# Performance work log

Hardware: AMD Instinct MI355X
Metric: run time of the kernel (lower is better)

Reference implementation:

```python
import jax, jax.numpy as jnp
import numpy as np

B, S, H, E = 2, 2048, 1024, 16


def setup_inputs() -> dict:
    key = jax.random.key(0)
    k0, k1, k2, k3 = jax.random.split(key, 4)
    tokens = jax.random.normal(k0, (B, S, H), dtype=jnp.float32)
    gate_w = jax.random.normal(k1, (E, H), dtype=jnp.float32) * (H ** -0.5)
    expert_w = jax.random.normal(k2, (E, H, H), dtype=jnp.float32) * (H ** -0.5)
    expert_b = jax.random.normal(k3, (E, H), dtype=jnp.float32) * 0.01
    return {"tokens": tokens, "gate_w": gate_w, "expert_w": expert_w, "expert_b": expert_b}


def reference(tokens, gate_w, expert_w, expert_b):
    b, s, h = tokens.shape
    # gate: Linear(H, E, bias=False) -> logits, softmax, top-2
    logits = jnp.einsum('bsh,eh->bse', tokens, gate_w)
    weights = jax.nn.softmax(logits, axis=-1)
    top2_w, top2_idx = jax.lax.top_k(weights, 2)           # [b,s,2]
    flat = tokens.reshape(b * s, h)                         # [N,H]
    flat_w = top2_w.reshape(b * s, 2)
    flat_idx = top2_idx.reshape(b * s, 2)
    # dense per-expert Linear+ReLU for all tokens (grouped GEMM form)
    y = jax.nn.relu(jnp.einsum('nh,edh->ned', flat, expert_w) + expert_b[None, :, :])  # [N,E,H]
    # gather the two selected experts per token and combine with gate weights
    sel = jnp.take_along_axis(y, flat_idx[:, :, None], axis=1)  # [N,2,H]
    out = jnp.sum(sel * flat_w[:, :, None], axis=1)             # [N,H]
    return out.reshape(b, s, h)
```

## Files before the change

kernel.cpp:

```cpp
#include <hip/hip_runtime.h>
#include <hip/hip_bf16.h>

#define TOKENS 4096
#define HDIM 1024
#define NEXP 16
#define BM 128
#define BN 128
#define BK 64
#define MAXMT (TOKENS / BM)

typedef __bf16 bf16x8 __attribute__((ext_vector_type(8)));
typedef __bf16 bf16x4 __attribute__((ext_vector_type(4)));
typedef float f32x4 __attribute__((ext_vector_type(4)));

__device__ inline void gload16(const void* g, const void* l) {
  __builtin_amdgcn_global_load_lds((const __attribute__((address_space(1))) void*)g,
                                   (__attribute__((address_space(3))) void*)l, 16, 0, 0);
}

#define WQ (NEXP * HDIM * HDIM / 4)
#define TQ (TOKENS * HDIM / 4)
__global__ __launch_bounds__(256) void convert_kernel(
    const float* __restrict__ w, const float* __restrict__ t,
    __bf16* __restrict__ wbf, __bf16* __restrict__ tbf) {
  int idx = blockIdx.x * 256 + threadIdx.x;
  for (int i = idx; i < WQ + TQ; i += gridDim.x * 256) {
    const float4* src;
    bf16x4* dst;
    int j;
    if (i < WQ) { src = (const float4*)w; dst = (bf16x4*)wbf; j = i; }
    else        { src = (const float4*)t; dst = (bf16x4*)tbf; j = i - WQ; }
    float4 f = src[j];
    bf16x4 v;
    v[0] = (__bf16)f.x; v[1] = (__bf16)f.y; v[2] = (__bf16)f.z; v[3] = (__bf16)f.w;
    dst[j] = v;
  }
}

__global__ __launch_bounds__(256) void gate_kernel(
    const float* __restrict__ tokens, const float* __restrict__ gate_w,
    int* __restrict__ tok_idx, float* __restrict__ tok_w) {
  int lane = threadIdx.x & 63;
  int wv = threadIdx.x >> 6;
  int token = blockIdx.x * 4 + wv;
  const float* trow = tokens + (size_t)token * HDIM;

  float4 tv[4];
#pragma unroll
  for (int s = 0; s < 4; ++s) tv[s] = *(const float4*)(trow + s * 256 + lane * 4);

  float lg[NEXP];
#pragma unroll
  for (int e = 0; e < NEXP; ++e) {
    float d = 0.f;
#pragma unroll
    for (int s = 0; s < 4; ++s) {
      float4 g = *(const float4*)(gate_w + e * HDIM + s * 256 + lane * 4);
      d += tv[s].x * g.x + tv[s].y * g.y + tv[s].z * g.z + tv[s].w * g.w;
    }
#pragma unroll
    for (int off = 32; off; off >>= 1) d += __shfl_xor(d, off);
    lg[e] = d;
  }

  int i0 = 0; float b0 = lg[0];
#pragma unroll
  for (int e = 1; e < NEXP; ++e) if (lg[e] > b0) { b0 = lg[e]; i0 = e; }
  int i1 = -1; float b1 = -1e30f;
#pragma unroll
  for (int e = 0; e < NEXP; ++e) {
    if (e == i0) continue;
    if (lg[e] > b1) { b1 = lg[e]; i1 = e; }
  }
  float s = 0.f;
#pragma unroll
  for (int e = 0; e < NEXP; ++e) s += expf(lg[e] - b0);
  float w0 = 1.0f / s;
  float w1 = expf(b1 - b0) / s;

  if (lane == 0) {
    tok_idx[token * 2 + 0] = i0;
    tok_idx[token * 2 + 1] = i1;
    tok_w[token * 2 + 0] = w0;
    tok_w[token * 2 + 1] = w1;
  }
}

__global__ __launch_bounds__(256) void build_lists_kernel(
    const int* __restrict__ tok_idx, const float* __restrict__ tok_w,
    int* __restrict__ counts, int* __restrict__ list_tok, float* __restrict__ list_w) {
  int e = blockIdx.x;
  __shared__ int cur;
  if (threadIdx.x == 0) cur = 0;
  __syncthreads();
  for (int s = threadIdx.x; s < TOKENS * 2; s += 256) {
    if (tok_idx[s] == e) {
      int pos = atomicAdd(&cur, 1);
      list_tok[e * TOKENS + pos] = s >> 1;
      list_w[e * TOKENS + pos] = tok_w[s];
    }
  }
  __syncthreads();
  if (threadIdx.x == 0) counts[e] = cur;
}

__global__ __launch_bounds__(256) void moe_gemm_kernel(
    const __bf16* __restrict__ tok_bf, const __bf16* __restrict__ w_bf,
    const float* __restrict__ expert_b, const int* __restrict__ counts,
    const int* __restrict__ list_tok, const float* __restrict__ list_w,
    float* __restrict__ out) {
  int e = blockIdx.x & 15;
  int mt = blockIdx.x >> 4;
  int cnt = counts[e];
  if (mt * BM >= cnt) return;
  int nt = blockIdx.y;
  const int lbase = e * TOKENS;

  __shared__ __bf16 lds[2][(BM + BN) * BK];

  int tid = threadIdx.x;
  int lane = tid & 63;
  int wv = tid >> 6;

  const __bf16* aptr[4];
  const __bf16* bptr[4];
  int dstb[4];
#pragma unroll
  for (int i = 0; i < 4; ++i) {
    int c = (wv * 4 + i) * 64 + lane;
    int r = c >> 3, kc = c & 7;
    int gr = mt * BM + r;
    int tok = list_tok[lbase + ((gr < cnt) ? gr : (cnt - 1))];
    aptr[i] = tok_bf + (size_t)tok * HDIM + (kc ^ (r & 7)) * 8;
    int d = nt * BN + r;
    bptr[i] = w_bf + (size_t)e * HDIM * HDIM + (size_t)d * HDIM + (kc ^ (r & 7)) * 8;
    dstb[i] = (wv * 4 + i) * 512;
  }

  int wr = (wv >> 1) * 64;
  int wc = (wv & 1) * 64;
  int lr = lane & 15;
  int lk = lane >> 4;

  int aoffr[2][4], boffr[2][4];
#pragma unroll
  for (int kk = 0; kk < 2; ++kk) {
#pragma unroll
    for (int m = 0; m < 4; ++m) {
      int r = wr + m * 16 + lr;
      aoffr[kk][m] = r * BK + (((kk * 4 + lk) ^ (r & 7)) * 8);
      int d = wc + m * 16 + lr;
      boffr[kk][m] = BM * BK + d * BK + (((kk * 4 + lk) ^ (d & 7)) * 8);
    }
  }

  f32x4 acc[4][4] = {};

#pragma unroll
  for (int i = 0; i < 4; ++i) gload16(aptr[i], &lds[0][dstb[i]]);
#pragma unroll
  for (int i = 0; i < 4; ++i) gload16(bptr[i], &lds[0][BM * BK + dstb[i]]);
  __syncthreads();

  int buf = 0;
  for (int kb = 0; kb < HDIM / BK; ++kb) {
    if (kb + 1 < HDIM / BK) {
      int nb = buf ^ 1;
      int ko = (kb + 1) * BK;
#pragma unroll
      for (int i = 0; i < 4; ++i) gload16(aptr[i] + ko, &lds[nb][dstb[i]]);
#pragma unroll
      for (int i = 0; i < 4; ++i) gload16(bptr[i] + ko, &lds[nb][BM * BK + dstb[i]]);
    }

    bf16x8 af[2][4], bfr[2][4];
#pragma unroll
    for (int kk = 0; kk < 2; ++kk) {
#pragma unroll
      for (int m = 0; m < 4; ++m) {
        af[kk][m] = *(const bf16x8*)(&lds[buf][aoffr[kk][m]]);
        bfr[kk][m] = *(const bf16x8*)(&lds[buf][boffr[kk][m]]);
      }
    }
#pragma unroll
    for (int kk = 0; kk < 2; ++kk)
#pragma unroll
      for (int m = 0; m < 4; ++m)
#pragma unroll
        for (int n = 0; n < 4; ++n)
          acc[m][n] = __builtin_amdgcn_mfma_f32_16x16x32_bf16(af[kk][m], bfr[kk][n], acc[m][n], 0, 0, 0);

    __syncthreads();
    buf ^= 1;
  }

#pragma unroll
  for (int m = 0; m < 4; ++m) {
#pragma unroll
    for (int j = 0; j < 4; ++j) {
      int rloc = wr + m * 16 + lk * 4 + j;
      int grow = mt * BM + rloc;
      if (grow < cnt) {
        int tok = list_tok[lbase + grow];
        float gw = list_w[lbase + grow];
        float* orow = out + (size_t)tok * HDIM + nt * BN + wc;
        const float* brow = expert_b + e * HDIM + nt * BN + wc;
#pragma unroll
        for (int n = 0; n < 4; ++n) {
          int dcol = n * 16 + lr;
          float v = acc[m][n][j] + brow[dcol];
          v = fmaxf(v, 0.f) * gw;
          atomicAdd(orow + dcol, v);
        }
      }
    }
  }
}

extern "C" void kernel_launch(void* const* d_in, const int* in_sizes, int n_in,
                              void* d_out, int out_size, void* d_ws, size_t ws_size,
                              hipStream_t stream) {
  const float* tokens = (const float*)d_in[0];
  const float* gate_w = (const float*)d_in[1];
  const float* expert_w = (const float*)d_in[2];
  const float* expert_b = (const float*)d_in[3];
  float* out = (float*)d_out;

  int* counts = (int*)d_ws;
  int* tok_idx = counts + 16;
  float* tok_w = (float*)(tok_idx + TOKENS * 2);
  int* list_tok = (int*)(tok_w + TOKENS * 2);
  float* list_w = (float*)(list_tok + NEXP * TOKENS);
  size_t head = (size_t)(list_w + NEXP * TOKENS) - (size_t)d_ws;
  head = (head + 255) & ~(size_t)255;
  __bf16* w_bf = (__bf16*)((char*)d_ws + head);
  __bf16* tok_bf = w_bf + (size_t)NEXP * HDIM * HDIM;

  hipMemsetAsync(d_out, 0, (size_t)out_size * sizeof(float), stream);

  convert_kernel<<<2048, 256, 0, stream>>>(expert_w, tokens, w_bf, tok_bf);
  gate_kernel<<<TOKENS / 4, 256, 0, stream>>>(tokens, gate_w, tok_idx, tok_w);
  build_lists_kernel<<<NEXP, 256, 0, stream>>>(tok_idx, tok_w, counts, list_tok, list_w);

  dim3 grid(NEXP * MAXMT, HDIM / BN);
  moe_gemm_kernel<<<grid, 256, 0, stream>>>(tok_bf, w_bf, expert_b, counts,
                                            list_tok, list_w, out);
}
```

Measured before the change: 236.9 us.

## Compact MoE tile schedule and use 512-thread GEMM blocks with split conversion

Adds a plan kernel that builds a compact list of (expert, m-tile) pairs, so GEMM blocks map only to real tiles instead of a sparse grid where most blocks exit early. The GEMM block grows to 512 threads (8 waves, each computing 64x32) with launch bounds for occupancy, and the fp32-to-bf16 conversion is split into two 8-wide vectorized kernels with one element group per thread. The cost is an extra single-thread serial kernel and launch, plus smaller per-wave tiles that reuse fragments less.

```diff
diff --git a/kernel.cpp b/kernel.cpp
--- a/kernel.cpp
+++ b/kernel.cpp
@@ -7,10 +7,9 @@
 #define BM 128
 #define BN 128
 #define BK 64
-#define MAXMT (TOKENS / BM)
+#define MAX_TILES (TOKENS * 2 / BM + NEXP)
 
 typedef __bf16 bf16x8 __attribute__((ext_vector_type(8)));
-typedef __bf16 bf16x4 __attribute__((ext_vector_type(4)));
 typedef float f32x4 __attribute__((ext_vector_type(4)));
 
 __device__ inline void gload16(const void* g, const void* l) {
@@ -18,23 +17,15 @@
                                    (__attribute__((address_space(3))) void*)l, 16, 0, 0);
 }
 
-#define WQ (NEXP * HDIM * HDIM / 4)
-#define TQ (TOKENS * HDIM / 4)
-__global__ __launch_bounds__(256) void convert_kernel(
-    const float* __restrict__ w, const float* __restrict__ t,
-    __bf16* __restrict__ wbf, __bf16* __restrict__ tbf) {
-  int idx = blockIdx.x * 256 + threadIdx.x;
-  for (int i = idx; i < WQ + TQ; i += gridDim.x * 256) {
-    const float4* src;
-    bf16x4* dst;
-    int j;
-    if (i < WQ) { src = (const float4*)w; dst = (bf16x4*)wbf; j = i; }
-    else        { src = (const float4*)t; dst = (bf16x4*)tbf; j = i - WQ; }
-    float4 f = src[j];
-    bf16x4 v;
-    v[0] = (__bf16)f.x; v[1] = (__bf16)f.y; v[2] = (__bf16)f.z; v[3] = (__bf16)f.w;
-    dst[j] = v;
-  }
+__global__ __launch_bounds__(256) void cvt_kernel(const float* __restrict__ src,
+                                                  __bf16* __restrict__ dst) {
+  int i = blockIdx.x * 256 + threadIdx.x;
+  float4 a = ((const float4*)src)[i * 2];
+  float4 b = ((const float4*)src)[i * 2 + 1];
+  bf16x8 v;
+  v[0] = (__bf16)a.x; v[1] = (__bf16)a.y; v[2] = (__bf16)a.z; v[3] = (__bf16)a.w;
+  v[4] = (__bf16)b.x; v[5] = (__bf16)b.y; v[6] = (__bf16)b.z; v[7] = (__bf16)b.w;
+  ((bf16x8*)dst)[i] = v;
 }
 
 __global__ __launch_bounds__(256) void gate_kernel(
@@ -104,15 +95,29 @@
   if (threadIdx.x == 0) counts[e] = cur;
 }
 
-__global__ __launch_bounds__(256) void moe_gemm_kernel(
+__global__ void plan_kernel(const int* __restrict__ counts, int* __restrict__ tiles,
+                            int* __restrict__ n_tiles) {
+  if (threadIdx.x == 0) {
+    int n = 0;
+    for (int e = 0; e < NEXP; ++e) {
+      int t = (counts[e] + BM - 1) / BM;
+      for (int m = 0; m < t; ++m) { tiles[n * 2] = e; tiles[n * 2 + 1] = m; ++n; }
+    }
+    *n_tiles = n;
+  }
+}
+
+__global__ __launch_bounds__(512, 4) void moe_gemm_kernel(
     const __bf16* __restrict__ tok_bf, const __bf16* __restrict__ w_bf,
     const float* __restrict__ expert_b, const int* __restrict__ counts,
+    const int* __restrict__ tiles, const int* __restrict__ n_tiles,
     const int* __restrict__ list_tok, const float* __restrict__ list_w,
     float* __restrict__ out) {
-  int e = blockIdx.x & 15;
-  int mt = blockIdx.x >> 4;
+  int bx = blockIdx.x;
+  if (bx >= *n_tiles) return;
+  int e = tiles[bx * 2];
+  int mt = tiles[bx * 2 + 1];
   int cnt = counts[e];
-  if (mt * BM >= cnt) return;
   int nt = blockIdx.y;
   const int lbase = e * TOKENS;
 
@@ -122,44 +127,47 @@
   int lane = tid & 63;
   int wv = tid >> 6;
 
-  const __bf16* aptr[4];
-  const __bf16* bptr[4];
-  int dstb[4];
-#pragma unroll
-  for (int i = 0; i < 4; ++i) {
-    int c = (wv * 4 + i) * 64 + lane;
+  const __bf16* aptr[2];
+  const __bf16* bptr[2];
+  int dstb[2];
+#pragma unroll
+  for (int i = 0; i < 2; ++i) {
+    int c = (wv * 2 + i) * 64 + lane;
     int r = c >> 3, kc = c & 7;
     int gr = mt * BM + r;
     int tok = list_tok[lbase + ((gr < cnt) ? gr : (cnt - 1))];
     aptr[i] = tok_bf + (size_t)tok * HDIM + (kc ^ (r & 7)) * 8;
     int d = nt * BN + r;
     bptr[i] = w_bf + (size_t)e * HDIM * HDIM + (size_t)d * HDIM + (kc ^ (r & 7)) * 8;
-    dstb[i] = (wv * 4 + i) * 512;
-  }
-
-  int wr = (wv >> 1) * 64;
-  int wc = (wv & 1) * 64;
+    dstb[i] = (wv * 2 + i) * 512;
+  }
+
+  int wr = (wv >> 2) * 64;
+  int wc = (wv & 3) * 32;
   int lr = lane & 15;
   int lk = lane >> 4;
 
-  int aoffr[2][4], boffr[2][4];
+  int aoffr[2][4], boffr[2][2];
 #pragma unroll
   for (int kk = 0; kk < 2; ++kk) {
 #pragma unroll
     for (int m = 0; m < 4; ++m) {
       int r = wr + m * 16 + lr;
       aoffr[kk][m] = r * BK + (((kk * 4 + lk) ^ (r & 7)) * 8);
-      int d = wc + m * 16 + lr;
-      boffr[kk][m] = BM * BK + d * BK + (((kk * 4 + lk) ^ (d & 7)) * 8);
-    }
-  }
-
-  f32x4 acc[4][4] = {};
-
-#pragma unroll
-  for (int i = 0; i < 4; ++i) gload16(aptr[i], &lds[0][dstb[i]]);
-#pragma unroll
-  for (int i = 0; i < 4; ++i) gload16(bptr[i], &lds[0][BM * BK + dstb[i]]);
+    }
+#pragma unroll
+    for (int n = 0; n < 2; ++n) {
+      int d = wc + n * 16 + lr;
+      boffr[kk][n] = BM * BK + d * BK + (((kk * 4 + lk) ^ (d & 7)) * 8);
+    }
+  }
+
+  f32x4 acc[4][2] = {};
+
+#pragma unroll
+  for (int i = 0; i < 2; ++i) gload16(aptr[i], &lds[0][dstb[i]]);
+#pragma unroll
+  for (int i = 0; i < 2; ++i) gload16(bptr[i], &lds[0][BM * BK + dstb[i]]);
   __syncthreads();
 
   int buf = 0;
@@ -168,26 +176,25 @@
       int nb = buf ^ 1;
       int ko = (kb + 1) * BK;
 #pragma unroll
-      for (int i = 0; i < 4; ++i) gload16(aptr[i] + ko, &lds[nb][dstb[i]]);
-#pragma unroll
-      for (int i = 0; i < 4; ++i) gload16(bptr[i] + ko, &lds[nb][BM * BK + dstb[i]]);
-    }
-
-    bf16x8 af[2][4], bfr[2][4];
+      for (int i = 0; i < 2; ++i) gload16(aptr[i] + ko, &lds[nb][dstb[i]]);
+#pragma unroll
+      for (int i = 0; i < 2; ++i) gload16(bptr[i] + ko, &lds[nb][BM * BK + dstb[i]]);
+    }
+
+    bf16x8 af[2][4], bfr[2][2];
 #pragma unroll
     for (int kk = 0; kk < 2; ++kk) {
 #pragma unroll
-      for (int m = 0; m < 4; ++m) {
-        af[kk][m] = *(const bf16x8*)(&lds[buf][aoffr[kk][m]]);
-        bfr[kk][m] = *(const bf16x8*)(&lds[buf][boffr[kk][m]]);
-      }
+      for (int m = 0; m < 4; ++m) af[kk][m] = *(const bf16x8*)(&lds[buf][aoffr[kk][m]]);
+#pragma unroll
+      for (int n = 0; n < 2; ++n) bfr[kk][n] = *(const bf16x8*)(&lds[buf][boffr[kk][n]]);
     }
 #pragma unroll
     for (int kk = 0; kk < 2; ++kk)
 #pragma unroll
       for (int m = 0; m < 4; ++m)
 #pragma unroll
-        for (int n = 0; n < 4; ++n)
+        for (int n = 0; n < 2; ++n)
           acc[m][n] = __builtin_amdgcn_mfma_f32_16x16x32_bf16(af[kk][m], bfr[kk][n], acc[m][n], 0, 0, 0);
 
     __syncthreads();
@@ -206,7 +213,7 @@
         float* orow = out + (size_t)tok * HDIM + nt * BN + wc;
         const float* brow = expert_b + e * HDIM + nt * BN + wc;
 #pragma unroll
-        for (int n = 0; n < 4; ++n) {
+        for (int n = 0; n < 2; ++n) {
           int dcol = n * 16 + lr;
           float v = acc[m][n][j] + brow[dcol];
           v = fmaxf(v, 0.f) * gw;
@@ -227,7 +234,9 @@
   float* out = (float*)d_out;
 
   int* counts = (int*)d_ws;
-  int* tok_idx = counts + 16;
+  int* n_tiles = counts + 16;
+  int* tiles = n_tiles + 16;
+  int* tok_idx = tiles + MAX_TILES * 2;
   float* tok_w = (float*)(tok_idx + TOKENS * 2);
   int* list_tok = (int*)(tok_w + TOKENS * 2);
   float* list_w = (float*)(list_tok + NEXP * TOKENS);
@@ -238,11 +247,13 @@
 
   hipMemsetAsync(d_out, 0, (size_t)out_size * sizeof(float), stream);
 
-  convert_kernel<<<2048, 256, 0, stream>>>(expert_w, tokens, w_bf, tok_bf);
+  cvt_kernel<<<NEXP * HDIM * HDIM / 8 / 256, 256, 0, stream>>>(expert_w, w_bf);
+  cvt_kernel<<<TOKENS * HDIM / 8 / 256, 256, 0, stream>>>(tokens, tok_bf);
   gate_kernel<<<TOKENS / 4, 256, 0, stream>>>(tokens, gate_w, tok_idx, tok_w);
   build_lists_kernel<<<NEXP, 256, 0, stream>>>(tok_idx, tok_w, counts, list_tok, list_w);
-
-  dim3 grid(NEXP * MAXMT, HDIM / BN);
-  moe_gemm_kernel<<<grid, 256, 0, stream>>>(tok_bf, w_bf, expert_b, counts,
+  plan_kernel<<<1, 64, 0, stream>>>(counts, tiles, n_tiles);
+
+  dim3 grid(MAX_TILES, HDIM / BN);
+  moe_gemm_kernel<<<grid, 512, 0, stream>>>(tok_bf, w_bf, expert_b, counts, tiles, n_tiles,
                                             list_tok, list_w, out);
 }
```

Result: faster. 227.7 us (-3.9%).

## Fuse weight bf16 conversion into GEMM with LDS-resident weight slab

Applied to the files above, without the earlier changes.

Removes the separate conversion kernel. The token bf16 cast moves into the gate kernel, and each GEMM block converts its own 64-column expert weight slice from fp32 into a full-K LDS slab (128KB). Each block then iterates over all of that expert's tokens, streaming A fragments straight from global memory with no LDS staging. This avoids writing and re-reading a bf16 copy of the weights, but the grid shrinks to 256 blocks, one per expert and column tile, so load imbalance across experts and uncoalesced direct A loads may limit throughput.

```diff
diff --git a/kernel.cpp b/kernel.cpp
--- a/kernel.cpp
+++ b/kernel.cpp
@@ -4,42 +4,18 @@
 #define TOKENS 4096
 #define HDIM 1024
 #define NEXP 16
-#define BM 128
-#define BN 128
-#define BK 64
-#define MAXMT (TOKENS / BM)
+#define BN 64
+#define NT (HDIM / BN)
+#define MGRP 5
+#define GP (8 * MGRP)
 
 typedef __bf16 bf16x8 __attribute__((ext_vector_type(8)));
 typedef __bf16 bf16x4 __attribute__((ext_vector_type(4)));
 typedef float f32x4 __attribute__((ext_vector_type(4)));
 
-__device__ inline void gload16(const void* g, const void* l) {
-  __builtin_amdgcn_global_load_lds((const __attribute__((address_space(1))) void*)g,
-                                   (__attribute__((address_space(3))) void*)l, 16, 0, 0);
-}
-
-#define WQ (NEXP * HDIM * HDIM / 4)
-#define TQ (TOKENS * HDIM / 4)
-__global__ __launch_bounds__(256) void convert_kernel(
-    const float* __restrict__ w, const float* __restrict__ t,
-    __bf16* __restrict__ wbf, __bf16* __restrict__ tbf) {
-  int idx = blockIdx.x * 256 + threadIdx.x;
-  for (int i = idx; i < WQ + TQ; i += gridDim.x * 256) {
-    const float4* src;
-    bf16x4* dst;
-    int j;
-    if (i < WQ) { src = (const float4*)w; dst = (bf16x4*)wbf; j = i; }
-    else        { src = (const float4*)t; dst = (bf16x4*)tbf; j = i - WQ; }
-    float4 f = src[j];
-    bf16x4 v;
-    v[0] = (__bf16)f.x; v[1] = (__bf16)f.y; v[2] = (__bf16)f.z; v[3] = (__bf16)f.w;
-    dst[j] = v;
-  }
-}
-
 __global__ __launch_bounds__(256) void gate_kernel(
     const float* __restrict__ tokens, const float* __restrict__ gate_w,
-    int* __restrict__ tok_idx, float* __restrict__ tok_w) {
+    int* __restrict__ tok_idx, float* __restrict__ tok_w, __bf16* __restrict__ tok_bf) {
   int lane = threadIdx.x & 63;
   int wv = threadIdx.x >> 6;
   int token = blockIdx.x * 4 + wv;
@@ -48,6 +24,14 @@
   float4 tv[4];
 #pragma unroll
   for (int s = 0; s < 4; ++s) tv[s] = *(const float4*)(trow + s * 256 + lane * 4);
+
+#pragma unroll
+  for (int s = 0; s < 4; ++s) {
+    bf16x4 v;
+    v[0] = (__bf16)tv[s].x; v[1] = (__bf16)tv[s].y;
+    v[2] = (__bf16)tv[s].z; v[3] = (__bf16)tv[s].w;
+    *(bf16x4*)(tok_bf + (size_t)token * HDIM + s * 256 + lane * 4) = v;
+  }
 
   float lg[NEXP];
 #pragma unroll
@@ -86,14 +70,14 @@
   }
 }
 
-__global__ __launch_bounds__(256) void build_lists_kernel(
+__global__ __launch_bounds__(1024) void build_lists_kernel(
     const int* __restrict__ tok_idx, const float* __restrict__ tok_w,
     int* __restrict__ counts, int* __restrict__ list_tok, float* __restrict__ list_w) {
   int e = blockIdx.x;
   __shared__ int cur;
   if (threadIdx.x == 0) cur = 0;
   __syncthreads();
-  for (int s = threadIdx.x; s < TOKENS * 2; s += 256) {
+  for (int s = threadIdx.x; s < TOKENS * 2; s += 1024) {
     if (tok_idx[s] == e) {
       int pos = atomicAdd(&cur, 1);
       list_tok[e * TOKENS + pos] = s >> 1;
@@ -104,113 +88,98 @@
   if (threadIdx.x == 0) counts[e] = cur;
 }
 
-__global__ __launch_bounds__(256) void moe_gemm_kernel(
-    const __bf16* __restrict__ tok_bf, const __bf16* __restrict__ w_bf,
+__global__ __launch_bounds__(512, 2) void moe_gemm_kernel(
+    const __bf16* __restrict__ tok_bf, const float* __restrict__ expert_w,
     const float* __restrict__ expert_b, const int* __restrict__ counts,
     const int* __restrict__ list_tok, const float* __restrict__ list_w,
     float* __restrict__ out) {
-  int e = blockIdx.x & 15;
-  int mt = blockIdx.x >> 4;
+  int e = blockIdx.x;
+  int nt = blockIdx.y;
   int cnt = counts[e];
-  if (mt * BM >= cnt) return;
-  int nt = blockIdx.y;
+  if (cnt == 0) return;
   const int lbase = e * TOKENS;
 
-  __shared__ __bf16 lds[2][(BM + BN) * BK];
+  __shared__ __bf16 Bl[BN * HDIM];
 
   int tid = threadIdx.x;
   int lane = tid & 63;
   int wv = tid >> 6;
 
-  const __bf16* aptr[4];
-  const __bf16* bptr[4];
-  int dstb[4];
-#pragma unroll
-  for (int i = 0; i < 4; ++i) {
-    int c = (wv * 4 + i) * 64 + lane;
-    int r = c >> 3, kc = c & 7;
-    int gr = mt * BM + r;
-    int tok = list_tok[lbase + ((gr < cnt) ? gr : (cnt - 1))];
-    aptr[i] = tok_bf + (size_t)tok * HDIM + (kc ^ (r & 7)) * 8;
-    int d = nt * BN + r;
-    bptr[i] = w_bf + (size_t)e * HDIM * HDIM + (size_t)d * HDIM + (kc ^ (r & 7)) * 8;
-    dstb[i] = (wv * 4 + i) * 512;
-  }
-
-  int wr = (wv >> 1) * 64;
-  int wc = (wv & 1) * 64;
+  {
+    const float* wbase = expert_w + ((size_t)e * HDIM + (size_t)nt * BN) * HDIM;
+#pragma unroll
+    for (int i = 0; i < 16; ++i) {
+      int c = i * 512 + tid;
+      int d = c >> 7, kc = c & 127;
+      const float* src = wbase + (size_t)d * HDIM + kc * 8;
+      float4 f0 = *(const float4*)(src);
+      float4 f1 = *(const float4*)(src + 4);
+      bf16x8 v;
+      v[0] = (__bf16)f0.x; v[1] = (__bf16)f0.y; v[2] = (__bf16)f0.z; v[3] = (__bf16)f0.w;
+      v[4] = (__bf16)f1.x; v[5] = (__bf16)f1.y; v[6] = (__bf16)f1.z; v[7] = (__bf16)f1.w;
+      *(bf16x8*)(&Bl[d * HDIM + ((kc ^ (d & 7)) * 8)]) = v;
+    }
+  }
+  __syncthreads();
+
   int lr = lane & 15;
   int lk = lane >> 4;
 
-  int aoffr[2][4], boffr[2][4];
-#pragma unroll
-  for (int kk = 0; kk < 2; ++kk) {
-#pragma unroll
-    for (int m = 0; m < 4; ++m) {
-      int r = wr + m * 16 + lr;
-      aoffr[kk][m] = r * BK + (((kk * 4 + lk) ^ (r & 7)) * 8);
-      int d = wc + m * 16 + lr;
-      boffr[kk][m] = BM * BK + d * BK + (((kk * 4 + lk) ^ (d & 7)) * 8);
-    }
-  }
-
-  f32x4 acc[4][4] = {};
-
-#pragma unroll
-  for (int i = 0; i < 4; ++i) gload16(aptr[i], &lds[0][dstb[i]]);
-#pragma unroll
-  for (int i = 0; i < 4; ++i) gload16(bptr[i], &lds[0][BM * BK + dstb[i]]);
-  __syncthreads();
-
-  int buf = 0;
-  for (int kb = 0; kb < HDIM / BK; ++kb) {
-    if (kb + 1 < HDIM / BK) {
-      int nb = buf ^ 1;
-      int ko = (kb + 1) * BK;
-#pragma unroll
-      for (int i = 0; i < 4; ++i) gload16(aptr[i] + ko, &lds[nb][dstb[i]]);
-#pragma unroll
-      for (int i = 0; i < 4; ++i) gload16(bptr[i] + ko, &lds[nb][BM * BK + dstb[i]]);
-    }
-
-    bf16x8 af[2][4], bfr[2][4];
-#pragma unroll
-    for (int kk = 0; kk < 2; ++kk) {
-#pragma unroll
-      for (int m = 0; m < 4; ++m) {
-        af[kk][m] = *(const bf16x8*)(&lds[buf][aoffr[kk][m]]);
-        bfr[kk][m] = *(const bf16x8*)(&lds[buf][boffr[kk][m]]);
+  int drow[4], dxor[4];
+#pragma unroll
+  for (int n = 0; n < 4; ++n) { int d = n * 16 + lr; drow[n] = d * HDIM; dxor[n] = d & 7; }
+
+  int ngroups = (cnt + 15) >> 4;
+  int npass = (ngroups + GP - 1) / GP;
+
+  for (int p = 0; p < npass; ++p) {
+    if (p * GP + wv >= ngroups) break;
+
+    int tok[MGRP];
+#pragma unroll
+    for (int i = 0; i < MGRP; ++i) {
+      int g = p * GP + i * 8 + wv;
+      int row = g * 16 + lr;
+      tok[i] = list_tok[lbase + min(row, cnt - 1)];
+    }
+
+    f32x4 acc[MGRP][4] = {};
+
+#pragma unroll 4
+    for (int kb = 0; kb < HDIM / 32; ++kb) {
+      bf16x8 a[MGRP], b[4];
+#pragma unroll
+      for (int i = 0; i < MGRP; ++i)
+        a[i] = *(const bf16x8*)(tok_bf + (size_t)tok[i] * HDIM + kb * 32 + lk * 8);
+#pragma unroll
+      for (int n = 0; n < 4; ++n) {
+        int kc = kb * 4 + lk;
+        b[n] = *(const bf16x8*)(&Bl[drow[n] + ((kc ^ dxor[n]) * 8)]);
       }
-    }
-#pragma unroll
-    for (int kk = 0; kk < 2; ++kk)
-#pragma unroll
-      for (int m = 0; m < 4; ++m)
+#pragma unroll
+      for (int i = 0; i < MGRP; ++i)
 #pragma unroll
         for (int n = 0; n < 4; ++n)
-          acc[m][n] = __builtin_amdgcn_mfma_f32_16x16x32_bf16(af[kk][m], bfr[kk][n], acc[m][n], 0, 0, 0);
-
-    __syncthreads();
-    buf ^= 1;
-  }
-
-#pragma unroll
-  for (int m = 0; m < 4; ++m) {
-#pragma unroll
-    for (int j = 0; j < 4; ++j) {
-      int rloc = wr + m * 16 + lk * 4 + j;
-      int grow = mt * BM + rloc;
-      if (grow < cnt) {
-        int tok = list_tok[lbase + grow];
-        float gw = list_w[lbase + grow];
-        float* orow = out + (size_t)tok * HDIM + nt * BN + wc;
-        const float* brow = expert_b + e * HDIM + nt * BN + wc;
+          acc[i][n] = __builtin_amdgcn_mfma_f32_16x16x32_bf16(a[i], b[n], acc[i][n], 0, 0, 0);
+    }
+
+    const float* brow = expert_b + e * HDIM + nt * BN;
+#pragma unroll
+    for (int i = 0; i < MGRP; ++i) {
+      int g = p * GP + i * 8 + wv;
+#pragma unroll
+      for (int j = 0; j < 4; ++j) {
+        int row = g * 16 + lk * 4 + j;
+        int cr = min(row, cnt - 1);
+        int tokr = list_tok[lbase + cr];
+        float gw = (row < cnt) ? list_w[lbase + row] : 0.f;
+        float* orow = out + (size_t)tokr * HDIM + nt * BN;
 #pragma unroll
         for (int n = 0; n < 4; ++n) {
-          int dcol = n * 16 + lr;
-          float v = acc[m][n][j] + brow[dcol];
+          int dc = n * 16 + lr;
+          float v = acc[i][n][j] + brow[dc];
           v = fmaxf(v, 0.f) * gw;
-          atomicAdd(orow + dcol, v);
+          atomicAdd(orow + dc, v);
         }
       }
     }
@@ -233,16 +202,14 @@
   float* list_w = (float*)(list_tok + NEXP * TOKENS);
   size_t head = (size_t)(list_w + NEXP * TOKENS) - (size_t)d_ws;
   head = (head + 255) & ~(size_t)255;
-  __bf16* w_bf = (__bf16*)((char*)d_ws + head);
-  __bf16* tok_bf = w_bf + (size_t)NEXP * HDIM * HDIM;
+  __bf16* tok_bf = (__bf16*)((char*)d_ws + head);
 
   hipMemsetAsync(d_out, 0, (size_t)out_size * sizeof(float), stream);
 
-  convert_kernel<<<2048, 256, 0, stream>>>(expert_w, tokens, w_bf, tok_bf);
-  gate_kernel<<<TOKENS / 4, 256, 0, stream>>>(tokens, gate_w, tok_idx, tok_w);
-  build_lists_kernel<<<NEXP, 256, 0, stream>>>(tok_idx, tok_w, counts, list_tok, list_w);
-
-  dim3 grid(NEXP * MAXMT, HDIM / BN);
-  moe_gemm_kernel<<<grid, 256, 0, stream>>>(tok_bf, w_bf, expert_b, counts,
+  gate_kernel<<<TOKENS / 4, 256, 0, stream>>>(tokens, gate_w, tok_idx, tok_w, tok_bf);
+  build_lists_kernel<<<NEXP, 1024, 0, stream>>>(tok_idx, tok_w, counts, list_tok, list_w);
+
+  dim3 grid(NEXP, NT);
+  moe_gemm_kernel<<<grid, 512, 0, stream>>>(tok_bf, expert_w, expert_b, counts,
                                             list_tok, list_w, out);
 }
```

Result: no change. 237.8 us (+0.4%).
